# Optimization experiments

Measured on AMD Instinct MI355X. Metric: run time of the kernel, lower is better.

## Reference

```python
import jax, jax.numpy as jnp
import numpy as np

N_HEADS = 12
HEAD_DIM = 64
EMB_DIM = 768
ATTN_DIM = N_HEADS * HEAD_DIM


def setup_inputs() -> dict:
    key = jax.random.key(0)
    k1, k2, k3, k4 = jax.random.split(key, 4)
    B, N = 8, 1024
    x = jax.random.normal(k1, (B, N, EMB_DIM), dtype=jnp.float32)
    scale = 1.0 / np.sqrt(EMB_DIM)
    w_qkv = jax.random.normal(k2, (EMB_DIM, 3 * ATTN_DIM), dtype=jnp.float32) * scale
    w_out = jax.random.normal(k3, (ATTN_DIM, EMB_DIM), dtype=jnp.float32) * (1.0 / np.sqrt(ATTN_DIM))
    b_out = jax.random.normal(k4, (EMB_DIM,), dtype=jnp.float32) * 0.01
    return {"x": x, "w_qkv": w_qkv, "w_out": w_out, "b_out": b_out}


def reference(x, w_qkv, w_out, b_out):
    B, N, _ = x.shape
    qkv = jnp.einsum('bnd,de->bne', x, w_qkv)  # [B,N,3*attn_dim]
    q, k, v = jnp.split(qkv, 3, axis=-1)
    # [B, n_heads, N, head_dim]
    def heads(t):
        return t.reshape(B, N, N_HEADS, HEAD_DIM).transpose(0, 2, 1, 3)
    q, k, v = heads(q), heads(k), heads(v)
    scores = jnp.einsum('bhnd,bhmd->bhnm', q, k) * (HEAD_DIM ** -0.5)
    attn = jax.nn.softmax(scores, axis=-1)
    out = jnp.einsum('bhnm,bhmd->bhnd', attn, v)
    out = out.transpose(0, 2, 1, 3).reshape(B, N, ATTN_DIM)
    return jnp.einsum('bnd,de->bne', out, w_out) + b_out
```

## Files before the change

### kernel.cpp

```cpp
#include <hip/hip_runtime.h>
#include <hip/hip_bf16.h>

typedef unsigned short u16;
typedef __attribute__((ext_vector_type(8))) short short8;
typedef __attribute__((ext_vector_type(4))) float floatx4;

#define SEQ    1024
#define EMB    768
#define NHEADS 12
#define HDIM   64
#define QKVD   2304
#define BATCH  8
#define ROWS   8192
#define QKW    1536

__device__ __forceinline__ u16 f2bf(float f) {
  unsigned int x; __builtin_memcpy(&x, &f, 4);
  x = (x + 0x7FFFu + ((x >> 16) & 1u)) >> 16;
  return (u16)x;
}
__device__ __forceinline__ u16 f2bf_t(float f) {
  unsigned int x; __builtin_memcpy(&x, &f, 4);
  return (u16)(x >> 16);
}

__device__ __forceinline__ void gld16(const void* g, void* l) {
  __builtin_amdgcn_global_load_lds(
      (const __attribute__((address_space(1))) void*)g,
      (__attribute__((address_space(3))) void*)l, 16, 0, 0);
}

__global__ __launch_bounds__(256) void f2bf_vec(const float* __restrict__ src,
                                                u16* __restrict__ dst, int n) {
  const int i = (blockIdx.x * 256 + threadIdx.x) * 8;
  if (i >= n) return;
  u16 tmp[8];
#pragma unroll
  for (int j = 0; j < 8; ++j) tmp[j] = f2bf(src[i + j]);
  *(uint4*)(dst + i) = *(const uint4*)tmp;
}

__global__ __launch_bounds__(256) void transpose_f2bf(const float* __restrict__ in,
                                                      u16* __restrict__ out,
                                                      int R, int C) {
  __shared__ u16 tile[32][33];
  const int c0 = blockIdx.x * 32, r0 = blockIdx.y * 32;
  const int tx = threadIdx.x, ty = threadIdx.y;
#pragma unroll
  for (int i = 0; i < 4; ++i)
    tile[ty + i * 8][tx] = f2bf(in[(size_t)(r0 + ty + i * 8) * C + c0 + tx]);
  __syncthreads();
#pragma unroll
  for (int i = 0; i < 4; ++i)
    out[(size_t)(c0 + ty + i * 8) * R + r0 + tx] = tile[tx][ty + i * 8];
}

__global__ __launch_bounds__(256) void gemm_qkv(const u16* __restrict__ A,
                                                const u16* __restrict__ Bt,
                                                u16* __restrict__ qk,
                                                u16* __restrict__ vT) {
  constexpr int K = EMB;
  __shared__ __align__(16) u16 As[128 * 64];
  __shared__ __align__(16) u16 Bs[128 * 64];
  const int t = threadIdx.x;
  const int w = t >> 6, lane = t & 63, l16 = lane & 15, quad = lane >> 4;
  const int wm = (w >> 1) * 64, wn = (w & 1) * 64;
  const int flat = blockIdx.y * 18 + blockIdx.x;
  const int grp = flat / 144, loc = flat % 144;
  const int m0 = (grp * 8 + (loc & 7)) * 128;
  const int n0 = (loc >> 3) * 128;

  floatx4 acc[4][4];
#pragma unroll
  for (int mt = 0; mt < 4; ++mt)
#pragma unroll
    for (int nt = 0; nt < 4; ++nt) acc[mt][nt] = (floatx4){0.f, 0.f, 0.f, 0.f};

  for (int k0 = 0; k0 < K; k0 += 64) {
    __syncthreads();
#pragma unroll
    for (int i = 0; i < 4; ++i) {
      const int idx = i * 256 + t;
      const int row = idx >> 3;
      const int gc8 = (((idx & 7) ^ (row & 7)) << 3);
      gld16(A  + (size_t)(m0 + row) * K + k0 + gc8, As + (size_t)idx * 8);
      gld16(Bt + (size_t)(n0 + row) * K + k0 + gc8, Bs + (size_t)idx * 8);
    }
    __syncthreads();

#pragma unroll
    for (int kk = 0; kk < 2; ++kk) {
      short8 a[4], b[4];
#pragma unroll
      for (int mt = 0; mt < 4; ++mt) {
        const int row = wm + mt * 16 + l16;
        a[mt] = *(const short8*)(As + row * 64 + ((((kk << 2) + quad) ^ (row & 7)) << 3));
      }
#pragma unroll
      for (int nt = 0; nt < 4; ++nt) {
        const int row = wn + nt * 16 + l16;
        b[nt] = *(const short8*)(Bs + row * 64 + ((((kk << 2) + quad) ^ (row & 7)) << 3));
      }
#pragma unroll
      for (int mt = 0; mt < 4; ++mt)
#pragma unroll
        for (int nt = 0; nt < 4; ++nt)
          acc[mt][nt] = __builtin_amdgcn_mfma_f32_16x16x32_bf16(a[mt], b[nt], acc[mt][nt], 0, 0, 0);
    }
  }

  if (n0 < QKW) {
#pragma unroll
    for (int mt = 0; mt < 4; ++mt)
#pragma unroll
      for (int nt = 0; nt < 4; ++nt) {
        const int col = n0 + wn + nt * 16 + l16;
#pragma unroll
        for (int r = 0; r < 4; ++r) {
          const int row = m0 + wm + mt * 16 + quad * 4 + r;
          qk[(size_t)row * QKW + col] = f2bf(acc[mt][nt][r]);
        }
      }
  } else {
#pragma unroll
    for (int mt = 0; mt < 4; ++mt) {
      const int rowb = m0 + wm + mt * 16 + quad * 4;
      const int b = rowb >> 10, n = rowb & 1023;
#pragma unroll
      for (int nt = 0; nt < 4; ++nt) {
        const int vc = n0 + wn + nt * 16 + l16 - QKW;
        const int h = vc >> 6, d = vc & 63;
        ushort4 pk;
        pk.x = f2bf(acc[mt][nt][0]); pk.y = f2bf(acc[mt][nt][1]);
        pk.z = f2bf(acc[mt][nt][2]); pk.w = f2bf(acc[mt][nt][3]);
        *(ushort4*)(vT + ((size_t)(b * NHEADS + h) * HDIM + d) * SEQ + n) = pk;
      }
    }
  }
}

__global__ __launch_bounds__(256) void flash_attn(const u16* __restrict__ qk,
                                                  const u16* __restrict__ vT,
                                                  u16* __restrict__ aout) {
  constexpr int LDF = 72;
  __shared__ __align__(16) u16 QPs[128 * LDF];
  __shared__ __align__(16) u16 Ks[64 * LDF];
  __shared__ __align__(16) u16 Vs[64 * LDF];

  const int t = threadIdx.x;
  const int w = t >> 6, lane = t & 63, l16 = lane & 15, quad = lane >> 4;
  const int bh = blockIdx.x, b = bh / NHEADS, h = bh % NHEADS;
  const int m0 = blockIdx.y * 128;
  constexpr float C_EXP = 0.125f * 1.44269504f;

  const size_t qbase = (size_t)(b * SEQ + m0) * QKW + h * HDIM;
#pragma unroll
  for (int i = 0; i < 4; ++i) {
    const int idx = i * 256 + t, row = idx >> 3, c8 = (idx & 7) << 3;
    *(uint4*)(QPs + row * LDF + c8) = *(const uint4*)(qk + qbase + (size_t)row * QKW + c8);
  }
  __syncthreads();

  short8 aq[2][2];
#pragma unroll
  for (int mt = 0; mt < 2; ++mt)
#pragma unroll
    for (int kk = 0; kk < 2; ++kk)
      aq[mt][kk] = *(const short8*)(QPs + (w * 32 + mt * 16 + l16) * LDF + kk * 32 + quad * 8);

  float l_r[2][4];
  floatx4 o[2][4];
#pragma unroll
  for (int mt = 0; mt < 2; ++mt)
#pragma unroll
    for (int r = 0; r < 4; ++r) l_r[mt][r] = 0.f;
#pragma unroll
  for (int mt = 0; mt < 2; ++mt)
#pragma unroll
    for (int ct = 0; ct < 4; ++ct) o[mt][ct] = (floatx4){0.f, 0.f, 0.f, 0.f};

  const size_t kbase = (size_t)(b * SEQ) * QKW + EMB + h * HDIM;
  const size_t vbase = (size_t)bh * HDIM * SEQ;
  u16* Pw = QPs + w * 32 * LDF;

  for (int n0 = 0; n0 < SEQ; n0 += 64) {
    __syncthreads();
#pragma unroll
    for (int i = 0; i < 2; ++i) {
      const int idx = i * 256 + t, kr = idx >> 3, c8 = (idx & 7) << 3;
      *(uint4*)(Ks + kr * LDF + c8) = *(const uint4*)(qk + kbase + (size_t)(n0 + kr) * QKW + c8);
      *(uint4*)(Vs + kr * LDF + c8) = *(const uint4*)(vT + vbase + (size_t)kr * SEQ + n0 + c8);
    }
    __syncthreads();

    floatx4 s[2][4];
#pragma unroll
    for (int mt = 0; mt < 2; ++mt)
#pragma unroll
      for (int nt = 0; nt < 4; ++nt) s[mt][nt] = (floatx4){0.f, 0.f, 0.f, 0.f};
#pragma unroll
    for (int nt = 0; nt < 4; ++nt) {
      const short8 bk0 = *(const short8*)(Ks + (nt * 16 + l16) * LDF + quad * 8);
      const short8 bk1 = *(const short8*)(Ks + (nt * 16 + l16) * LDF + 32 + quad * 8);
#pragma unroll
      for (int mt = 0; mt < 2; ++mt) {
        s[mt][nt] = __builtin_amdgcn_mfma_f32_16x16x32_bf16(aq[mt][0], bk0, s[mt][nt], 0, 0, 0);
        s[mt][nt] = __builtin_amdgcn_mfma_f32_16x16x32_bf16(aq[mt][1], bk1, s[mt][nt], 0, 0, 0);
      }
    }

#pragma unroll
    for (int mt = 0; mt < 2; ++mt)
#pragma unroll
      for (int r = 0; r < 4; ++r) {
        float p0 = __builtin_exp2f(s[mt][0][r] * C_EXP);
        float p1 = __builtin_exp2f(s[mt][1][r] * C_EXP);
        float p2 = __builtin_exp2f(s[mt][2][r] * C_EXP);
        float p3 = __builtin_exp2f(s[mt][3][r] * C_EXP);
        l_r[mt][r] += (p0 + p1) + (p2 + p3);
        u16* pr = Pw + (mt * 16 + quad * 4 + r) * LDF + l16;
        pr[0]  = f2bf_t(p0);
        pr[16] = f2bf_t(p1);
        pr[32] = f2bf_t(p2);
        pr[48] = f2bf_t(p3);
      }

#pragma unroll
    for (int kk = 0; kk < 2; ++kk) {
      const short8 ap0 = *(const short8*)(Pw + (0 * 16 + l16) * LDF + kk * 32 + quad * 8);
      const short8 ap1 = *(const short8*)(Pw + (1 * 16 + l16) * LDF + kk * 32 + quad * 8);
#pragma unroll
      for (int ct = 0; ct < 4; ++ct) {
        const short8 bv = *(const short8*)(Vs + (ct * 16 + l16) * LDF + kk * 32 + quad * 8);
        o[0][ct] = __builtin_amdgcn_mfma_f32_16x16x32_bf16(ap0, bv, o[0][ct], 0, 0, 0);
        o[1][ct] = __builtin_amdgcn_mfma_f32_16x16x32_bf16(ap1, bv, o[1][ct], 0, 0, 0);
      }
    }
  }

  float inv[2][4];
#pragma unroll
  for (int mt = 0; mt < 2; ++mt)
#pragma unroll
    for (int r = 0; r < 4; ++r) {
      float l = l_r[mt][r];
      l += __shfl_xor(l, 1);
      l += __shfl_xor(l, 2);
      l += __shfl_xor(l, 4);
      l += __shfl_xor(l, 8);
      inv[mt][r] = 1.f / l;
    }
#pragma unroll
  for (int mt = 0; mt < 2; ++mt)
#pragma unroll
    for (int ct = 0; ct < 4; ++ct)
#pragma unroll
      for (int r = 0; r < 4; ++r) {
        const int row = m0 + w * 32 + mt * 16 + quad * 4 + r;
        const int col = h * HDIM + ct * 16 + l16;
        aout[(size_t)(b * SEQ + row) * EMB + col] = f2bf(o[mt][ct][r] * inv[mt][r]);
      }
}

__global__ __launch_bounds__(256) void gemm_out(const u16* __restrict__ A,
                                                const u16* __restrict__ Bt,
                                                const float* __restrict__ bias,
                                                float* __restrict__ C) {
  constexpr int K = EMB, N = EMB;
  __shared__ __align__(16) u16 As[64 * 64];
  __shared__ __align__(16) u16 Bs[128 * 64];
  const int t = threadIdx.x;
  const int w = t >> 6, lane = t & 63, l16 = lane & 15, quad = lane >> 4;
  const int wm = (w >> 1) * 32, wn = (w & 1) * 64;
  const int flat = blockIdx.y * 6 + blockIdx.x;
  const int grp = flat / 48, loc = flat % 48;
  const int m0 = (grp * 8 + (loc & 7)) * 64;
  const int n0 = (loc >> 3) * 128;

  floatx4 acc[2][4];
#pragma unroll
  for (int mt = 0; mt < 2; ++mt)
#pragma unroll
    for (int nt = 0; nt < 4; ++nt) acc[mt][nt] = (floatx4){0.f, 0.f, 0.f, 0.f};

  for (int k0 = 0; k0 < K; k0 += 64) {
    __syncthreads();
#pragma unroll
    for (int i = 0; i < 2; ++i) {
      const int idx = i * 256 + t;
      const int row = idx >> 3;
      const int gc8 = (((idx & 7) ^ (row & 7)) << 3);
      gld16(A + (size_t)(m0 + row) * K + k0 + gc8, As + (size_t)idx * 8);
    }
#pragma unroll
    for (int i = 0; i < 4; ++i) {
      const int idx = i * 256 + t;
      const int row = idx >> 3;
      const int gc8 = (((idx & 7) ^ (row & 7)) << 3);
      gld16(Bt + (size_t)(n0 + row) * K + k0 + gc8, Bs + (size_t)idx * 8);
    }
    __syncthreads();

#pragma unroll
    for (int kk = 0; kk < 2; ++kk) {
      short8 a[2], b[4];
#pragma unroll
      for (int mt = 0; mt < 2; ++mt) {
        const int row = wm + mt * 16 + l16;
        a[mt] = *(const short8*)(As + row * 64 + ((((kk << 2) + quad) ^ (row & 7)) << 3));
      }
#pragma unroll
      for (int nt = 0; nt < 4; ++nt) {
        const int row = wn + nt * 16 + l16;
        b[nt] = *(const short8*)(Bs + row * 64 + ((((kk << 2) + quad) ^ (row & 7)) << 3));
      }
#pragma unroll
      for (int mt = 0; mt < 2; ++mt)
#pragma unroll
        for (int nt = 0; nt < 4; ++nt)
          acc[mt][nt] = __builtin_amdgcn_mfma_f32_16x16x32_bf16(a[mt], b[nt], acc[mt][nt], 0, 0, 0);
    }
  }

#pragma unroll
  for (int mt = 0; mt < 2; ++mt)
#pragma unroll
    for (int nt = 0; nt < 4; ++nt) {
      const int col = n0 + wn + nt * 16 + l16;
      const float badd = bias[col];
#pragma unroll
      for (int r = 0; r < 4; ++r) {
        const int row = m0 + wm + mt * 16 + quad * 4 + r;
        C[(size_t)row * N + col] = acc[mt][nt][r] + badd;
      }
    }
}

extern "C" void kernel_launch(void* const* d_in, const int* in_sizes, int n_in,
                              void* d_out, int out_size, void* d_ws, size_t ws_size,
                              hipStream_t stream) {
  const float* x     = (const float*)d_in[0];
  const float* w_qkv = (const float*)d_in[1];
  const float* w_out = (const float*)d_in[2];
  const float* b_out = (const float*)d_in[3];
  float* out = (float*)d_out;

  u16* qk    = (u16*)d_ws;
  u16* vT    = qk    + (size_t)ROWS * QKW;
  u16* xb    = vT    + (size_t)BATCH * NHEADS * HDIM * SEQ;
  u16* aout  = xb;
  u16* wqkvT = xb    + (size_t)ROWS * EMB;
  u16* woutT = wqkvT + (size_t)QKVD * EMB;

  f2bf_vec<<<ROWS * EMB / 8 / 256, 256, 0, stream>>>(x, xb, ROWS * EMB);
  transpose_f2bf<<<dim3(QKVD / 32, EMB / 32), dim3(32, 8), 0, stream>>>(w_qkv, wqkvT, EMB, QKVD);
  transpose_f2bf<<<dim3(EMB / 32, EMB / 32), dim3(32, 8), 0, stream>>>(w_out, woutT, EMB, EMB);

  gemm_qkv<<<dim3(18, 64), 256, 0, stream>>>(xb, wqkvT, qk, vT);

  flash_attn<<<dim3(BATCH * NHEADS, SEQ / 128), 256, 0, stream>>>(qk, vT, aout);

  gemm_out<<<dim3(6, 128), 256, 0, stream>>>(aout, woutT, b_out, out);
}
```

Measured before the change: 208.6 us.

## Swizzle flash-attn LDS, compute transposed scores, async K/V loads

Replaces the padded LDS layout in the attention kernel with an XOR-swizzled unpadded layout, and loads K/V tiles directly into LDS with global_load_lds. Scores are computed transposed (K as A operand, Q as B), so each lane holds four consecutive keys. P can then be written as packed 64-bit stores instead of scalar u16 stores, and the row-sum reduction shrinks to two cross-quad shuffles. It also switches to the raw hardware exp2 intrinsic. The intent is to cut LDS bank conflicts, store instruction count and load latency, at the cost of more intricate indexing.

Measured after the change: 194.8 us. 1.07x faster.

```diff
diff --git a/kernel.cpp b/kernel.cpp
--- a/kernel.cpp
+++ b/kernel.cpp
@@ -19,9 +19,10 @@
   x = (x + 0x7FFFu + ((x >> 16) & 1u)) >> 16;
   return (u16)x;
 }
-__device__ __forceinline__ u16 f2bf_t(float f) {
-  unsigned int x; __builtin_memcpy(&x, &f, 4);
-  return (u16)(x >> 16);
+__device__ __forceinline__ unsigned int pack2bf_t(float a, float b) {
+  unsigned int ua, ub;
+  __builtin_memcpy(&ua, &a, 4); __builtin_memcpy(&ub, &b, 4);
+  return (ub & 0xFFFF0000u) | (ua >> 16);
 }
 
 __device__ __forceinline__ void gld16(const void* g, void* l) {
@@ -142,10 +143,9 @@
 __global__ __launch_bounds__(256) void flash_attn(const u16* __restrict__ qk,
                                                   const u16* __restrict__ vT,
                                                   u16* __restrict__ aout) {
-  constexpr int LDF = 72;
-  __shared__ __align__(16) u16 QPs[128 * LDF];
-  __shared__ __align__(16) u16 Ks[64 * LDF];
-  __shared__ __align__(16) u16 Vs[64 * LDF];
+  __shared__ __align__(16) u16 QPs[128 * 64];
+  __shared__ __align__(16) u16 Ks[64 * 64];
+  __shared__ __align__(16) u16 Vs[64 * 64];
 
   const int t = threadIdx.x;
   const int w = t >> 6, lane = t & 63, l16 = lane & 15, quad = lane >> 4;
@@ -156,24 +156,22 @@
   const size_t qbase = (size_t)(b * SEQ + m0) * QKW + h * HDIM;
 #pragma unroll
   for (int i = 0; i < 4; ++i) {
-    const int idx = i * 256 + t, row = idx >> 3, c8 = (idx & 7) << 3;
-    *(uint4*)(QPs + row * LDF + c8) = *(const uint4*)(qk + qbase + (size_t)row * QKW + c8);
+    const int idx = i * 256 + t, row = idx >> 3, c = idx & 7;
+    *(uint4*)(QPs + row * 64 + ((c ^ (row & 7)) << 3)) =
+        *(const uint4*)(qk + qbase + (size_t)row * QKW + (c << 3));
   }
   __syncthreads();
 
-  short8 aq[2][2];
-#pragma unroll
-  for (int mt = 0; mt < 2; ++mt)
-#pragma unroll
-    for (int kk = 0; kk < 2; ++kk)
-      aq[mt][kk] = *(const short8*)(QPs + (w * 32 + mt * 16 + l16) * LDF + kk * 32 + quad * 8);
-
-  float l_r[2][4];
+  short8 bq[2][2];
+#pragma unroll
+  for (int mt = 0; mt < 2; ++mt)
+#pragma unroll
+    for (int kc = 0; kc < 2; ++kc)
+      bq[mt][kc] = *(const short8*)(QPs + (w * 32 + mt * 16 + l16) * 64 +
+                                    ((((kc << 2) + quad) ^ (l16 & 7)) << 3));
+
+  float l_r[2] = {0.f, 0.f};
   floatx4 o[2][4];
-#pragma unroll
-  for (int mt = 0; mt < 2; ++mt)
-#pragma unroll
-    for (int r = 0; r < 4; ++r) l_r[mt][r] = 0.f;
 #pragma unroll
   for (int mt = 0; mt < 2; ++mt)
 #pragma unroll
@@ -181,75 +179,79 @@
 
   const size_t kbase = (size_t)(b * SEQ) * QKW + EMB + h * HDIM;
   const size_t vbase = (size_t)bh * HDIM * SEQ;
-  u16* Pw = QPs + w * 32 * LDF;
+  u16* Pw = QPs + w * 32 * 64;
 
   for (int n0 = 0; n0 < SEQ; n0 += 64) {
     __syncthreads();
 #pragma unroll
     for (int i = 0; i < 2; ++i) {
-      const int idx = i * 256 + t, kr = idx >> 3, c8 = (idx & 7) << 3;
-      *(uint4*)(Ks + kr * LDF + c8) = *(const uint4*)(qk + kbase + (size_t)(n0 + kr) * QKW + c8);
-      *(uint4*)(Vs + kr * LDF + c8) = *(const uint4*)(vT + vbase + (size_t)kr * SEQ + n0 + c8);
-    }
-    __syncthreads();
-
-    floatx4 s[2][4];
-#pragma unroll
-    for (int mt = 0; mt < 2; ++mt)
-#pragma unroll
-      for (int nt = 0; nt < 4; ++nt) s[mt][nt] = (floatx4){0.f, 0.f, 0.f, 0.f};
-#pragma unroll
-    for (int nt = 0; nt < 4; ++nt) {
-      const short8 bk0 = *(const short8*)(Ks + (nt * 16 + l16) * LDF + quad * 8);
-      const short8 bk1 = *(const short8*)(Ks + (nt * 16 + l16) * LDF + 32 + quad * 8);
+      const int idx = i * 256 + t, kr = idx >> 3;
+      const int gc = (((idx & 7) ^ (kr & 7)) << 3);
+      gld16(qk + kbase + (size_t)(n0 + kr) * QKW + gc, Ks + (size_t)idx * 8);
+      gld16(vT + vbase + (size_t)kr * SEQ + n0 + gc,   Vs + (size_t)idx * 8);
+    }
+    __syncthreads();
+
+    floatx4 st[4][2];
+#pragma unroll
+    for (int kt = 0; kt < 4; ++kt)
+#pragma unroll
+      for (int mt = 0; mt < 2; ++mt) st[kt][mt] = (floatx4){0.f, 0.f, 0.f, 0.f};
+#pragma unroll
+    for (int kt = 0; kt < 4; ++kt) {
+      const int krow = (kt * 16 + l16) * 64;
+      const short8 ak0 = *(const short8*)(Ks + krow + (((0 + quad) ^ (l16 & 7)) << 3));
+      const short8 ak1 = *(const short8*)(Ks + krow + (((4 + quad) ^ (l16 & 7)) << 3));
 #pragma unroll
       for (int mt = 0; mt < 2; ++mt) {
-        s[mt][nt] = __builtin_amdgcn_mfma_f32_16x16x32_bf16(aq[mt][0], bk0, s[mt][nt], 0, 0, 0);
-        s[mt][nt] = __builtin_amdgcn_mfma_f32_16x16x32_bf16(aq[mt][1], bk1, s[mt][nt], 0, 0, 0);
-      }
-    }
-
-#pragma unroll
-    for (int mt = 0; mt < 2; ++mt)
-#pragma unroll
-      for (int r = 0; r < 4; ++r) {
-        float p0 = __builtin_exp2f(s[mt][0][r] * C_EXP);
-        float p1 = __builtin_exp2f(s[mt][1][r] * C_EXP);
-        float p2 = __builtin_exp2f(s[mt][2][r] * C_EXP);
-        float p3 = __builtin_exp2f(s[mt][3][r] * C_EXP);
-        l_r[mt][r] += (p0 + p1) + (p2 + p3);
-        u16* pr = Pw + (mt * 16 + quad * 4 + r) * LDF + l16;
-        pr[0]  = f2bf_t(p0);
-        pr[16] = f2bf_t(p1);
-        pr[32] = f2bf_t(p2);
-        pr[48] = f2bf_t(p3);
-      }
+        st[kt][mt] = __builtin_amdgcn_mfma_f32_16x16x32_bf16(ak0, bq[mt][0], st[kt][mt], 0, 0, 0);
+        st[kt][mt] = __builtin_amdgcn_mfma_f32_16x16x32_bf16(ak1, bq[mt][1], st[kt][mt], 0, 0, 0);
+      }
+    }
+
+#pragma unroll
+    for (int mt = 0; mt < 2; ++mt) {
+      float lacc = 0.f;
+#pragma unroll
+      for (int kt = 0; kt < 4; ++kt) {
+        const float p0 = __builtin_amdgcn_exp2f(st[kt][mt][0] * C_EXP);
+        const float p1 = __builtin_amdgcn_exp2f(st[kt][mt][1] * C_EXP);
+        const float p2 = __builtin_amdgcn_exp2f(st[kt][mt][2] * C_EXP);
+        const float p3 = __builtin_amdgcn_exp2f(st[kt][mt][3] * C_EXP);
+        lacc += (p0 + p1) + (p2 + p3);
+        uint2 pw2;
+        pw2.x = pack2bf_t(p0, p1);
+        pw2.y = pack2bf_t(p2, p3);
+        *(uint2*)(Pw + (mt * 16 + l16) * 64 +
+                  ((((kt << 1) + (quad >> 1)) ^ (l16 & 7)) << 3) + (quad & 1) * 4) = pw2;
+      }
+      l_r[mt] += lacc;
+    }
 
 #pragma unroll
     for (int kk = 0; kk < 2; ++kk) {
-      const short8 ap0 = *(const short8*)(Pw + (0 * 16 + l16) * LDF + kk * 32 + quad * 8);
-      const short8 ap1 = *(const short8*)(Pw + (1 * 16 + l16) * LDF + kk * 32 + quad * 8);
+      const int sl = (((kk << 2) + quad) ^ (l16 & 7)) << 3;
+      const short8 ap0 = *(const short8*)(Pw + (0 * 16 + l16) * 64 + sl);
+      const short8 ap1 = *(const short8*)(Pw + (1 * 16 + l16) * 64 + sl);
 #pragma unroll
       for (int ct = 0; ct < 4; ++ct) {
-        const short8 bv = *(const short8*)(Vs + (ct * 16 + l16) * LDF + kk * 32 + quad * 8);
+        const short8 bv = *(const short8*)(Vs + (ct * 16 + l16) * 64 + sl);
         o[0][ct] = __builtin_amdgcn_mfma_f32_16x16x32_bf16(ap0, bv, o[0][ct], 0, 0, 0);
         o[1][ct] = __builtin_amdgcn_mfma_f32_16x16x32_bf16(ap1, bv, o[1][ct], 0, 0, 0);
       }
     }
   }
 
-  float inv[2][4];
-#pragma unroll
-  for (int mt = 0; mt < 2; ++mt)
-#pragma unroll
-    for (int r = 0; r < 4; ++r) {
-      float l = l_r[mt][r];
-      l += __shfl_xor(l, 1);
-      l += __shfl_xor(l, 2);
-      l += __shfl_xor(l, 4);
-      l += __shfl_xor(l, 8);
-      inv[mt][r] = 1.f / l;
-    }
+  float invs[2][4];
+#pragma unroll
+  for (int mt = 0; mt < 2; ++mt) {
+    float l = l_r[mt];
+    l += __shfl_xor(l, 16);
+    l += __shfl_xor(l, 32);
+    const float iv = 1.f / l;
+#pragma unroll
+    for (int r = 0; r < 4; ++r) invs[mt][r] = __shfl(iv, quad * 4 + r);
+  }
 #pragma unroll
   for (int mt = 0; mt < 2; ++mt)
 #pragma unroll
@@ -258,7 +260,7 @@
       for (int r = 0; r < 4; ++r) {
         const int row = m0 + w * 32 + mt * 16 + quad * 4 + r;
         const int col = h * HDIM + ct * 16 + l16;
-        aout[(size_t)(b * SEQ + row) * EMB + col] = f2bf(o[mt][ct][r] * inv[mt][r]);
+        aout[(size_t)(b * SEQ + row) * EMB + col] = f2bf(o[mt][ct][r] * invs[mt][r]);
       }
 }
 
```
